# Optimization experiments

Measured on AMD Instinct MI355X. Metric: run time of the kernel, lower is better.

## Reference

```python
import jax, jax.numpy as jnp
import numpy as np
from jax import lax

LSTM_UNITS = 64
BATCH = 2048
TIMESTEPS = 1024


def _lstm_cell(x, h, c, W_ih, W_hh, b_ih, b_hh):
    # PyTorch LSTMCell gate order: i, f, g, o
    gates = x @ W_ih.T + b_ih + h @ W_hh.T + b_hh
    i, f, g, o = jnp.split(gates, 4, axis=-1)
    c_new = jax.nn.sigmoid(f) * c + jax.nn.sigmoid(i) * jnp.tanh(g)
    h_new = jax.nn.sigmoid(o) * jnp.tanh(c_new)
    return h_new, c_new


def setup_inputs() -> dict:
    key = jax.random.key(0)
    ks = jax.random.split(key, 9)
    U = LSTM_UNITS
    s0 = 1.0 / np.sqrt(U)  # torch LSTMCell init scale (hidden=64)
    s1 = 1.0  # hidden=1 -> scale 1/sqrt(1)
    inp = {
        "input": jax.random.normal(ks[0], (BATCH, TIMESTEPS), dtype=jnp.float32),
        # c0: LSTMCell(1, 64)
        "W_ih0": jax.random.uniform(ks[1], (4 * U, 1), jnp.float32, -s0, s0),
        "W_hh0": jax.random.uniform(ks[2], (4 * U, U), jnp.float32, -s0, s0),
        "b_ih0": jax.random.uniform(ks[3], (4 * U,), jnp.float32, -s0, s0),
        "b_hh0": jax.random.uniform(ks[4], (4 * U,), jnp.float32, -s0, s0),
        # c1: LSTMCell(64, 1)
        "W_ih1": jax.random.uniform(ks[5], (4, U), jnp.float32, -s1, s1),
        "W_hh1": jax.random.uniform(ks[6], (4, 1), jnp.float32, -s1, s1),
        "b_ih1": jax.random.uniform(ks[7], (4,), jnp.float32, -s1, s1),
        "b_hh1": jax.random.uniform(ks[8], (4,), jnp.float32, -s1, s1),
    }
    return inp


def reference(input, W_ih0, W_hh0, b_ih0, b_hh0, W_ih1, W_hh1, b_ih1, b_hh1):
    B = input.shape[0]
    U = LSTM_UNITS
    dt = input.dtype
    h0 = jnp.zeros((B, U), dt)
    c0 = jnp.zeros((B, U), dt)
    h1 = jnp.zeros((B, 1), dt)
    c1 = jnp.zeros((B, 1), dt)

    def step(carry, x_t):
        h0, c0, h1, c1 = carry
        h0n, c0n = _lstm_cell(x_t, h0, c0, W_ih0, W_hh0, b_ih0, b_hh0)
        # NOTE: the original feeds the CELL state c0n (not h0n) into layer 2
        h1n, c1n = _lstm_cell(c0n, h1, c1, W_ih1, W_hh1, b_ih1, b_hh1)
        # output per step is the cell state of layer 2
        return (h0n, c0n, h1n, c1n), c1n

    xs = input.T[:, :, None]  # (T, B, 1)
    _, ys = lax.scan(step, (h0, c0, h1, c1), xs)  # ys: (T, B, 1)
    return ys[:, :, 0].T  # (B, T)
```

## Files before the change

### kernel.cpp

```cpp
#include <hip/hip_runtime.h>

#define T_STEPS 1024
#define BATCH 2048
#define BTILE 8
#define HS 36

typedef short short8 __attribute__((ext_vector_type(8)));
typedef float f32x4 __attribute__((ext_vector_type(4)));
typedef float f32x2 __attribute__((ext_vector_type(2)));

__device__ __forceinline__ float fast_rcp(float x) {
#if __has_builtin(__builtin_amdgcn_rcpf)
    return __builtin_amdgcn_rcpf(x);
#else
    return 1.0f / x;
#endif
}

__device__ __forceinline__ float fast_exp2(float x) {
#if __has_builtin(__builtin_amdgcn_exp2f)
    return __builtin_amdgcn_exp2f(x);
#else
    return exp2f(x);
#endif
}

__device__ __forceinline__ float sigf(float x) {
    return fast_rcp(1.0f + fast_exp2(-1.44269504f * x));
}

__device__ __forceinline__ f32x2 sigf2(f32x2 v) {
    f32x2 t = v * (-1.44269504f);
    f32x2 e = {fast_exp2(t[0]), fast_exp2(t[1])};
    e = e + 1.0f;
    return f32x2{fast_rcp(e[0]), fast_rcp(e[1])};
}

__device__ __forceinline__ float tanh_fast(float x) {
    float e = fast_exp2(2.88539008f * x);
    return 1.0f - 2.0f * fast_rcp(e + 1.0f);
}

__device__ __forceinline__ f32x2 tanh2(f32x2 v) {
    f32x2 t = v * 2.88539008f;
    f32x2 e = {fast_exp2(t[0]), fast_exp2(t[1])};
    e = e + 1.0f;
    f32x2 r = {fast_rcp(e[0]), fast_rcp(e[1])};
    return f32x2{1.0f, 1.0f} - 2.0f * r;
}

__device__ __forceinline__ unsigned f2bf(float x) {
    unsigned u = __float_as_uint(x);
    unsigned r = u + 0x7FFFu + ((u >> 16) & 1u);
    return r >> 16;
}

__device__ __forceinline__ unsigned cvt_pk_bf16(float a, float b) {
    unsigned r;
    asm("v_cvt_pk_bf16_f32 %0, %1, %2" : "=v"(r) : "v"(a), "v"(b));
    return r;
}

__device__ __forceinline__ void step_barrier() {
    asm volatile("s_waitcnt lgkmcnt(0)\n\ts_barrier" ::: "memory");
}

__global__ __launch_bounds__(320, 1)
void lstm_v14_kernel(const float* __restrict__ input,
                     const float* __restrict__ W_ih0,
                     const float* __restrict__ W_hh0,
                     const float* __restrict__ b_ih0,
                     const float* __restrict__ b_hh0,
                     const float* __restrict__ W_ih1,
                     const float* __restrict__ W_hh1,
                     const float* __restrict__ b_ih1,
                     const float* __restrict__ b_hh1,
                     float* __restrict__ out)
{
    const int tid = threadIdx.x;
    const int w8  = tid >> 6;
    const int l   = tid & 63;
    const int q16 = l >> 4;
    const int n16 = l & 15;
    const int n8  = l & 7;
    const int hi8 = n16 >> 3;
    const int ua  = 16 * w8 + 4 * q16 + 2 * hi8;
    const int bbase = blockIdx.x * BTILE;

    __shared__ __align__(16) unsigned Hbuf[2][16][HS];
    __shared__ float Xb[2][BTILE][65];
    __shared__ __align__(16) f32x4 Pbuf[2][8][8];

    for (int i = tid; i < 2 * 16 * HS; i += 320)
        reinterpret_cast<unsigned*>(Hbuf)[i] = 0u;

    short8 a1[4][2];
    f32x2 wg2[4], bg2[4];
    float w1A[4], w1B[4];
    if (w8 < 4) {
        #pragma unroll
        for (int g = 0; g < 4; ++g) {
            #pragma unroll
            for (int kt = 0; kt < 2; ++kt) {
                const float* p = W_hh0 + (size_t)(16 * (w8 + 4 * g) + n16) * 64 + kt * 32 + q16 * 8;
                short8 a;
                #pragma unroll
                for (int j = 0; j < 8; ++j) a[j] = (short)f2bf(p[j]);
                a1[g][kt] = a;
            }
        }
        #pragma unroll
        for (int g = 0; g < 4; ++g) {
            int rA = g * 64 + ua;
            int rB = rA + 1;
            wg2[g] = f32x2{W_ih0[rA], W_ih0[rB]};
            bg2[g] = f32x2{b_ih0[rA] + b_hh0[rA], b_ih0[rB] + b_hh0[rB]};
            w1A[g] = W_ih1[g * 64 + ua];
            w1B[g] = W_ih1[g * 64 + ua + 1];
        }
    }
    float wh1[4], bb1[4];
    #pragma unroll
    for (int g = 0; g < 4; ++g) { wh1[g] = W_hh1[g]; bb1[g] = b_ih1[g] + b_hh1[g]; }

    const int xr = (tid >> 5) & 7;
    const int xc = tid & 31;
    const float* rowptr = input + (size_t)(bbase + xr) * T_STEPS;
    if (tid < 256) {
        Xb[0][xr][xc]      = rowptr[xc];
        Xb[0][xr][xc + 32] = rowptr[xc + 32];
    }
    float xnA = 0.0f, xnB = 0.0f;
    f32x2 c02 = {0.0f, 0.0f};
    float h1 = 0.0f, c1 = 0.0f;

    __syncthreads();

    int par = 0;
    #pragma unroll 2
    for (int t = 0; t < T_STEPS; ++t) {
        if (w8 < 4) {
            if ((t & 63) == 0 && t + 64 < T_STEPS) {
                xnA = rowptr[t + 64 + xc];
                xnB = rowptr[t + 64 + xc + 32];
            }
            const int cp = (t >> 6) & 1;

            const unsigned* Hrow = &Hbuf[par][n16][0];
            short8 hb0 = *reinterpret_cast<const short8*>(Hrow + 4 * q16);
            short8 hb1 = *reinterpret_cast<const short8*>(Hrow + 16 + 4 * q16);

            f32x4 accv[4];
            #pragma unroll
            for (int g = 0; g < 4; ++g) {
                f32x4 z = {0.0f, 0.0f, 0.0f, 0.0f};
                z = __builtin_amdgcn_mfma_f32_16x16x32_bf16(a1[g][0], hb0, z, 0, 0, 0);
                z = __builtin_amdgcn_mfma_f32_16x16x32_bf16(a1[g][1], hb1, z, 0, 0, 0);
                accv[g] = z;
            }

            float vA[4], vB[4];
            #pragma unroll
            for (int g = 0; g < 4; ++g) {
                int pa = __float_as_int(accv[g][0]);
                pa = __builtin_amdgcn_update_dpp(pa, __float_as_int(accv[g][2]), 0x118, 0xf, 0xC, false);
                int pb = __float_as_int(accv[g][1]);
                pb = __builtin_amdgcn_update_dpp(pb, __float_as_int(accv[g][3]), 0x118, 0xf, 0xC, false);
                vA[g] = __int_as_float(pa);
                vB[g] = __int_as_float(pb);
            }

            float x = Xb[cp][n8][t & 63];
            f32x2 xx = {x, x};
            f32x2 gi = f32x2{vA[0], vB[0]} + (xx * wg2[0] + bg2[0]);
            f32x2 gf = f32x2{vA[1], vB[1]} + (xx * wg2[1] + bg2[1]);
            f32x2 gg = f32x2{vA[2], vB[2]} + (xx * wg2[2] + bg2[2]);
            f32x2 go = f32x2{vA[3], vB[3]} + (xx * wg2[3] + bg2[3]);

            f32x2 si = sigf2(gi);
            f32x2 sf = sigf2(gf);
            f32x2 tg = tanh2(gg);
            f32x2 c0n2 = sf * c02 + si * tg;
            c02 = c0n2;
            f32x2 so = sigf2(go);
            f32x2 th = tanh2(c0n2);
            f32x2 h0n2 = so * th;

            const int widx = 8 * w8 + 2 * q16 + hi8;
            Hbuf[par ^ 1][n8][widx] = cvt_pk_bf16(h0n2[0], h0n2[1]);

            float pg[4];
            #pragma unroll
            for (int g = 0; g < 4; ++g)
                pg[g] = w1A[g] * c0n2[0] + w1B[g] * c0n2[1];
            #pragma unroll
            for (int g = 0; g < 4; ++g) {
                float s = pg[g] + __int_as_float(
                    __builtin_amdgcn_ds_swizzle(__float_as_int(pg[g]), 0x201F));
                s = s + __int_as_float(
                    __builtin_amdgcn_ds_swizzle(__float_as_int(s), 0x401F));
                pg[g] = s;
            }
            if ((l & 31) < 8) {
                const int pslot = 2 * w8 + (l >> 5);
                Pbuf[par ^ 1][pslot][n8] = f32x4{pg[0], pg[1], pg[2], pg[3]};
            }

            if ((t & 63) == 63 && t + 1 < T_STEPS) {
                Xb[cp ^ 1][xr][xc]      = xnA;
                Xb[cp ^ 1][xr][xc + 32] = xnB;
            }
        } else {
            if (t > 0 && l < 8) {
                f32x4 s = Pbuf[par][0][l];
                #pragma unroll
                for (int p = 1; p < 8; ++p) s += Pbuf[par][p][l];
                float gi = s[0] + bb1[0] + h1 * wh1[0];
                float gf = s[1] + bb1[1] + h1 * wh1[1];
                float gg = s[2] + bb1[2] + h1 * wh1[2];
                float go = s[3] + bb1[3] + h1 * wh1[3];
                float c1n = sigf(gf) * c1 + sigf(gi) * tanh_fast(gg);
                c1 = c1n;
                h1 = sigf(go) * tanh_fast(c1n);
                out[(size_t)(bbase + l) * T_STEPS + (t - 1)] = c1n;
            }
        }

        step_barrier();
        par ^= 1;
    }

    if (w8 == 4 && l < 8) {
        f32x4 s = Pbuf[par][0][l];
        #pragma unroll
        for (int p = 1; p < 8; ++p) s += Pbuf[par][p][l];
        float gi = s[0] + bb1[0] + h1 * wh1[0];
        float gf = s[1] + bb1[1] + h1 * wh1[1];
        float gg = s[2] + bb1[2] + h1 * wh1[2];
        float c1n = sigf(gf) * c1 + sigf(gi) * tanh_fast(gg);
        out[(size_t)(bbase + l) * T_STEPS + (T_STEPS - 1)] = c1n;
    }
}

extern "C" void kernel_launch(void* const* d_in, const int* in_sizes, int n_in,
                              void* d_out, int out_size, void* d_ws, size_t ws_size,
                              hipStream_t stream) {
    const float* input = (const float*)d_in[0];
    const float* W_ih0 = (const float*)d_in[1];
    const float* W_hh0 = (const float*)d_in[2];
    const float* b_ih0 = (const float*)d_in[3];
    const float* b_hh0 = (const float*)d_in[4];
    const float* W_ih1 = (const float*)d_in[5];
    const float* W_hh1 = (const float*)d_in[6];
    const float* b_ih1 = (const float*)d_in[7];
    const float* b_hh1 = (const float*)d_in[8];
    float* out = (float*)d_out;

    lstm_v14_kernel<<<dim3(BATCH / BTILE), dim3(320), 0, stream>>>(
        input, W_ih0, W_hh0, b_ih0, b_hh0, W_ih1, W_hh1, b_ih1, b_hh1, out);
}
```

Before: 523.5 us.

## Defer layer-2 partial reduction by one step to overlap with MFMA latency

The cross-lane reduction and LDS store of the layer-2 gate partial sums move from the tail of each step to just after the next step's MFMA issue, so they hide behind MFMA latency instead of sitting on the critical path before the barrier. The layer-2 wave now consumes partials two steps late, and a drain epilogue handles the last two timesteps. The first butterfly stage also switches from ds_swizzle to a DPP row xor, avoiding an LDS-path op. This adds an extra barrier and epilogue code, and relies on correct Pbuf double-buffer indexing across the skewed schedule.

```diff
diff --git a/kernel.cpp b/kernel.cpp
--- a/kernel.cpp
+++ b/kernel.cpp
@@ -61,12 +61,16 @@
     return r;
 }
 
+__device__ __forceinline__ float dpp_xor8(float v) {
+    return __int_as_float(__builtin_amdgcn_update_dpp(0, __float_as_int(v), 0x128, 0xf, 0xf, true));
+}
+
 __device__ __forceinline__ void step_barrier() {
     asm volatile("s_waitcnt lgkmcnt(0)\n\ts_barrier" ::: "memory");
 }
 
 __global__ __launch_bounds__(320, 1)
-void lstm_v14_kernel(const float* __restrict__ input,
+void lstm_v15_kernel(const float* __restrict__ input,
                      const float* __restrict__ W_ih0,
                      const float* __restrict__ W_hh0,
                      const float* __restrict__ b_ih0,
@@ -133,6 +137,7 @@
     float xnA = 0.0f, xnB = 0.0f;
     f32x2 c02 = {0.0f, 0.0f};
     float h1 = 0.0f, c1 = 0.0f;
+    float pgc[4] = {0.0f, 0.0f, 0.0f, 0.0f};
 
     __syncthreads();
 
@@ -157,6 +162,20 @@
                 z = __builtin_amdgcn_mfma_f32_16x16x32_bf16(a1[g][0], hb0, z, 0, 0, 0);
                 z = __builtin_amdgcn_mfma_f32_16x16x32_bf16(a1[g][1], hb1, z, 0, 0, 0);
                 accv[g] = z;
+            }
+
+            if (t > 0) {
+                #pragma unroll
+                for (int g = 0; g < 4; ++g) {
+                    float s = pgc[g] + dpp_xor8(pgc[g]);
+                    s = s + __int_as_float(
+                        __builtin_amdgcn_ds_swizzle(__float_as_int(s), 0x401F));
+                    pgc[g] = s;
+                }
+                if ((l & 31) < 8) {
+                    const int pslot = 2 * w8 + (l >> 5);
+                    Pbuf[(t - 1) & 1][pslot][n8] = f32x4{pgc[0], pgc[1], pgc[2], pgc[3]};
+                }
             }
 
             float vA[4], vB[4];
@@ -189,32 +208,19 @@
             const int widx = 8 * w8 + 2 * q16 + hi8;
             Hbuf[par ^ 1][n8][widx] = cvt_pk_bf16(h0n2[0], h0n2[1]);
 
-            float pg[4];
             #pragma unroll
             for (int g = 0; g < 4; ++g)
-                pg[g] = w1A[g] * c0n2[0] + w1B[g] * c0n2[1];
-            #pragma unroll
-            for (int g = 0; g < 4; ++g) {
-                float s = pg[g] + __int_as_float(
-                    __builtin_amdgcn_ds_swizzle(__float_as_int(pg[g]), 0x201F));
-                s = s + __int_as_float(
-                    __builtin_amdgcn_ds_swizzle(__float_as_int(s), 0x401F));
-                pg[g] = s;
-            }
-            if ((l & 31) < 8) {
-                const int pslot = 2 * w8 + (l >> 5);
-                Pbuf[par ^ 1][pslot][n8] = f32x4{pg[0], pg[1], pg[2], pg[3]};
-            }
+                pgc[g] = w1A[g] * c0n2[0] + w1B[g] * c0n2[1];
 
             if ((t & 63) == 63 && t + 1 < T_STEPS) {
                 Xb[cp ^ 1][xr][xc]      = xnA;
                 Xb[cp ^ 1][xr][xc + 32] = xnB;
             }
         } else {
-            if (t > 0 && l < 8) {
-                f32x4 s = Pbuf[par][0][l];
+            if (t > 1 && l < 8) {
+                f32x4 s = Pbuf[t & 1][0][l];
                 #pragma unroll
-                for (int p = 1; p < 8; ++p) s += Pbuf[par][p][l];
+                for (int p = 1; p < 8; ++p) s += Pbuf[t & 1][p][l];
                 float gi = s[0] + bb1[0] + h1 * wh1[0];
                 float gf = s[1] + bb1[1] + h1 * wh1[1];
                 float gg = s[2] + bb1[2] + h1 * wh1[2];
@@ -222,7 +228,7 @@
                 float c1n = sigf(gf) * c1 + sigf(gi) * tanh_fast(gg);
                 c1 = c1n;
                 h1 = sigf(go) * tanh_fast(c1n);
-                out[(size_t)(bbase + l) * T_STEPS + (t - 1)] = c1n;
+                out[(size_t)(bbase + l) * T_STEPS + (t - 2)] = c1n;
             }
         }
 
@@ -230,15 +236,45 @@
         par ^= 1;
     }
 
+    if (w8 < 4) {
+        #pragma unroll
+        for (int g = 0; g < 4; ++g) {
+            float s = pgc[g] + dpp_xor8(pgc[g]);
+            s = s + __int_as_float(
+                __builtin_amdgcn_ds_swizzle(__float_as_int(s), 0x401F));
+            pgc[g] = s;
+        }
+        if ((l & 31) < 8) {
+            const int pslot = 2 * w8 + (l >> 5);
+            Pbuf[1][pslot][n8] = f32x4{pgc[0], pgc[1], pgc[2], pgc[3]};
+        }
+    }
+    step_barrier();
+
     if (w8 == 4 && l < 8) {
-        f32x4 s = Pbuf[par][0][l];
-        #pragma unroll
-        for (int p = 1; p < 8; ++p) s += Pbuf[par][p][l];
-        float gi = s[0] + bb1[0] + h1 * wh1[0];
-        float gf = s[1] + bb1[1] + h1 * wh1[1];
-        float gg = s[2] + bb1[2] + h1 * wh1[2];
-        float c1n = sigf(gf) * c1 + sigf(gi) * tanh_fast(gg);
-        out[(size_t)(bbase + l) * T_STEPS + (T_STEPS - 1)] = c1n;
+        {
+            f32x4 s = Pbuf[0][0][l];
+            #pragma unroll
+            for (int p = 1; p < 8; ++p) s += Pbuf[0][p][l];
+            float gi = s[0] + bb1[0] + h1 * wh1[0];
+            float gf = s[1] + bb1[1] + h1 * wh1[1];
+            float gg = s[2] + bb1[2] + h1 * wh1[2];
+            float go = s[3] + bb1[3] + h1 * wh1[3];
+            float c1n = sigf(gf) * c1 + sigf(gi) * tanh_fast(gg);
+            c1 = c1n;
+            h1 = sigf(go) * tanh_fast(c1n);
+            out[(size_t)(bbase + l) * T_STEPS + (T_STEPS - 2)] = c1n;
+        }
+        {
+            f32x4 s = Pbuf[1][0][l];
+            #pragma unroll
+            for (int p = 1; p < 8; ++p) s += Pbuf[1][p][l];
+            float gi = s[0] + bb1[0] + h1 * wh1[0];
+            float gf = s[1] + bb1[1] + h1 * wh1[1];
+            float gg = s[2] + bb1[2] + h1 * wh1[2];
+            float c1n = sigf(gf) * c1 + sigf(gi) * tanh_fast(gg);
+            out[(size_t)(bbase + l) * T_STEPS + (T_STEPS - 1)] = c1n;
+        }
     }
 }
 
@@ -256,6 +292,6 @@
     const float* b_hh1 = (const float*)d_in[8];
     float* out = (float*)d_out;
 
-    lstm_v14_kernel<<<dim3(BATCH / BTILE), dim3(320), 0, stream>>>(
+    lstm_v15_kernel<<<dim3(BATCH / BTILE), dim3(320), 0, stream>>>(
         input, W_ih0, W_hh0, b_ih0, b_hh0, W_ih1, W_hh1, b_ih1, b_hh1, out);
 }
```

After: 552.3 us. 5.5% more time.
